# Kernel optimization log

Hardware: AMD Instinct MI355X
Metric: run time of the kernel (lower is better)

The kernel has to match this reference:

```python
import jax, jax.numpy as jnp
import numpy as np

T = 16384
D = 2048      # input_dim
H = 256       # gru hidden
NF = 8        # n_frames (top-k)
NC = 2        # n_classes


def _gru_dir(x_gates, W_hh, b_hh, reverse):
    # x_gates: (T, 3H) precomputed input projection; torch gate order: r, z, n
    def step(h, gx):
        gh = h @ W_hh.T + b_hh
        xr, xz, xn = jnp.split(gx, 3)
        hr, hz, hn = jnp.split(gh, 3)
        r = jax.nn.sigmoid(xr + hr)
        z = jax.nn.sigmoid(xz + hz)
        n = jnp.tanh(xn + r * hn)
        h_new = (1.0 - z) * n + z * h
        return h_new, h_new
    h0 = jnp.zeros((W_hh.shape[1],), x_gates.dtype)
    _, hs = jax.lax.scan(step, h0, x_gates, reverse=reverse)
    return hs  # (T, H)


def setup_inputs() -> dict:
    key = jax.random.key(0)
    ks = jax.random.split(key, 16)
    s = 0.02
    inp = {
        "features": jax.random.normal(ks[0], (T, D), jnp.float32),
        "temperature": jnp.float32(0.5),
        # BiGRU params (torch layout: W_ih (3H, D), W_hh (3H, H))
        "W_ih_f": jax.random.normal(ks[1], (3 * H, D), jnp.float32) * s,
        "W_hh_f": jax.random.normal(ks[2], (3 * H, H), jnp.float32) * s,
        "b_ih_f": jnp.zeros((3 * H,), jnp.float32),
        "b_hh_f": jnp.zeros((3 * H,), jnp.float32),
        "W_ih_b": jax.random.normal(ks[3], (3 * H, D), jnp.float32) * s,
        "W_hh_b": jax.random.normal(ks[4], (3 * H, H), jnp.float32) * s,
        "b_ih_b": jnp.zeros((3 * H,), jnp.float32),
        "b_hh_b": jnp.zeros((3 * H,), jnp.float32),
        # scorer MLP: Linear(2H,64) -> ReLU -> Linear(64,1)
        "Ws1": jax.random.normal(ks[5], (64, 2 * H), jnp.float32) * s,
        "bs1": jnp.zeros((64,), jnp.float32),
        "Ws2": jax.random.normal(ks[6], (1, 64), jnp.float32) * s,
        "bs2": jnp.zeros((1,), jnp.float32),
        # classifier: Linear(D,256) -> ReLU -> Linear(256,NC)
        "Wc1": jax.random.normal(ks[7], (256, D), jnp.float32) * s,
        "bc1": jnp.zeros((256,), jnp.float32),
        "Wc2": jax.random.normal(ks[8], (NC, 256), jnp.float32) * s,
        "bc2": jnp.zeros((NC,), jnp.float32),
    }
    return inp


def reference(features, temperature, W_ih_f, W_hh_f, b_ih_f, b_hh_f,
              W_ih_b, W_hh_b, b_ih_b, b_hh_b, Ws1, bs1, Ws2, bs2,
              Wc1, bc1, Wc2, bc2):
    # FrameScorer: BiGRU
    gx_f = features @ W_ih_f.T + b_ih_f            # (T, 3H)
    gx_b = features @ W_ih_b.T + b_ih_b
    h_f = _gru_dir(gx_f, W_hh_f, b_hh_f, reverse=False)
    h_b = _gru_dir(gx_b, W_hh_b, b_hh_b, reverse=True)
    h = jnp.concatenate([h_f, h_b], axis=-1)       # (T, 2H)
    # scorer MLP (dropout is identity in eval)
    scores = (jax.nn.relu(h @ Ws1.T + bs1) @ Ws2.T + bs2)[:, 0]   # (T,)
    # soft top-k weights
    n = min(NF, scores.shape[0])
    _, topk_idx = jax.lax.top_k(scores, n)
    mask = jnp.zeros_like(scores).at[topk_idx].set(1.0)
    masked_scores = scores * mask + (1.0 - mask) * (-1e9)
    weights = jax.nn.softmax(masked_scores / temperature)          # (T,)
    # weighted feature sum + classifier
    clip_repr = weights @ features                                  # (D,)
    logits = jax.nn.relu(clip_repr @ Wc1.T + bc1) @ Wc2.T + bc2     # (NC,)
    return logits, scores
```

## Files before the change

### kernel.cpp

```cpp
#include <hip/hip_runtime.h>
#include <hip/hip_fp16.h>
#include <math.h>

#define T_LEN 16384
#define D_IN  2048
#define H_GRU 256
#define G3    768
#define NFRM  8
#define NCLS  2

#define CHUNK 32
#define WARM  48
#define GSTEPS (WARM + CHUNK)
#define BQ    4
#define NCHUNK (T_LEN / CHUNK)
#define GRU_BLOCKS (NCHUNK / BQ)

typedef _Float16 f16x8 __attribute__((ext_vector_type(8)));
typedef float    f32x4 __attribute__((ext_vector_type(4)));

static const size_t OFF_GXF = 0;
static const size_t OFF_GXB = OFF_GXF + (size_t)T_LEN * G3;
static const size_t OFF_H   = OFF_GXB + (size_t)T_LEN * G3;
static const size_t OFF_BIA = OFF_H   + (size_t)T_LEN * 512;
static const size_t OFF_SC  = OFF_BIA + 2 * G3;
static const size_t OFF_WPF = OFF_SC  + (size_t)T_LEN;
static const size_t OFF_WPB = OFF_WPF + (size_t)G3 * H_GRU / 2;
static const size_t OFF_SEL = OFF_WPB + (size_t)G3 * H_GRU / 2;
static const size_t OFF_CH  = OFF_SEL + 16;

__device__ __forceinline__ float fsig(float x) {
    return __builtin_amdgcn_rcpf(1.f + __expf(-x));
}
__device__ __forceinline__ float ftanh(float x) {
    float e = __expf(2.f * x);
    return 1.f - 2.f * __builtin_amdgcn_rcpf(e + 1.f);
}

__global__ void bias_fold_kernel(const float* __restrict__ bi0, const float* __restrict__ bh0,
                                 const float* __restrict__ bi1, const float* __restrict__ bh1,
                                 float* __restrict__ o0, float* __restrict__ o1) {
    int t = blockIdx.x * 256 + threadIdx.x;
    if (t < G3) {
        float a0 = bi0[t], a1 = bi1[t];
        if (t < 512) { a0 += bh0[t]; a1 += bh1[t]; }
        o0[t] = a0; o1[t] = a1;
    }
}

__global__ void pack_whh_mfma_kernel(const float* __restrict__ W0,
                                     const float* __restrict__ W1,
                                     f16x8* __restrict__ P0,
                                     f16x8* __restrict__ P1) {
    const float* W = blockIdx.y ? W1 : W0;
    f16x8* P = blockIdx.y ? P1 : P0;
    int tc = blockIdx.x;
    int l = threadIdx.x;
    int t = tc >> 3, c = tc & 7;
    int m = t * 16 + (l & 15);
    int k = c * 32 + (l >> 4) * 8;
    const float* src = W + (size_t)m * H_GRU + k;
    f16x8 v;
#pragma unroll
    for (int j = 0; j < 8; ++j) v[j] = (_Float16)src[j];
    P[(size_t)tc * 64 + l] = v;
}

#define GM 128
#define GN 128
#define GK 32
__global__ __launch_bounds__(256, 2) void gemm_f16_kernel(
    const float* __restrict__ A,
    const float* __restrict__ B0, const float* __restrict__ B1,
    const float* __restrict__ bias0, const float* __restrict__ bias1,
    float* __restrict__ C0, float* __restrict__ C1,
    int M, int N, int K) {
    const float* __restrict__ B    = blockIdx.z ? B1 : B0;
    const float* __restrict__ bias = blockIdx.z ? bias1 : bias0;
    float* __restrict__ C          = blockIdx.z ? C1 : C0;

    __shared__ __align__(16) __half As[GM][GK];
    __shared__ __align__(16) __half Bs[GN][GK];

    const int tid  = threadIdx.x;
    const int bm   = blockIdx.x * GM;
    const int bn   = blockIdx.y * GN;
    const int lane = tid & 63;
    const int wave = tid >> 6;
    const int mw   = wave & 1;
    const int nw   = wave >> 1;
    const int lm   = lane & 15;
    const int lk   = lane >> 4;

    const int srow = tid >> 3;
    const int scol = (tid & 7) * 4;

    f32x4 acc[4][4];
#pragma unroll
    for (int a = 0; a < 4; ++a)
#pragma unroll
        for (int b = 0; b < 4; ++b) acc[a][b] = (f32x4)0.f;

    for (int k0 = 0; k0 < K; k0 += GK) {
        float4 av[4], bv[4];
#pragma unroll
        for (int j = 0; j < 4; ++j) {
            av[j] = *(const float4*)&A[(size_t)(bm + 32 * j + srow) * K + k0 + scol];
            bv[j] = *(const float4*)&B[(size_t)(bn + 32 * j + srow) * K + k0 + scol];
        }
        __syncthreads();
#pragma unroll
        for (int j = 0; j < 4; ++j) {
            int r = 32 * j + srow;
            *((__half2*)&As[r][scol + 0]) = __float22half2_rn(make_float2(av[j].x, av[j].y));
            *((__half2*)&As[r][scol + 2]) = __float22half2_rn(make_float2(av[j].z, av[j].w));
            *((__half2*)&Bs[r][scol + 0]) = __float22half2_rn(make_float2(bv[j].x, bv[j].y));
            *((__half2*)&Bs[r][scol + 2]) = __float22half2_rn(make_float2(bv[j].z, bv[j].w));
        }
        __syncthreads();

        f16x8 afr[4], bfr[4];
#pragma unroll
        for (int tm = 0; tm < 4; ++tm)
            afr[tm] = *(const f16x8*)&As[64 * mw + 16 * tm + lm][lk * 8];
#pragma unroll
        for (int tn = 0; tn < 4; ++tn)
            bfr[tn] = *(const f16x8*)&Bs[64 * nw + 16 * tn + lm][lk * 8];
#pragma unroll
        for (int tm = 0; tm < 4; ++tm)
#pragma unroll
            for (int tn = 0; tn < 4; ++tn)
                acc[tm][tn] = __builtin_amdgcn_mfma_f32_16x16x32_f16(
                    afr[tm], bfr[tn], acc[tm][tn], 0, 0, 0);
    }

#pragma unroll
    for (int tm = 0; tm < 4; ++tm) {
#pragma unroll
        for (int tn = 0; tn < 4; ++tn) {
            int gn = bn + 64 * nw + 16 * tn + lm;
            float bb = bias[gn];
#pragma unroll
            for (int reg = 0; reg < 4; ++reg) {
                int gm = bm + 64 * mw + 16 * tm + lk * 4 + reg;
                C[(size_t)gm * N + gn] = acc[tm][tn][reg] + bb;
            }
        }
    }
}

#define BM 64
#define BN 64
#define BK 32
__global__ __launch_bounds__(256) void scorer_kernel(
    const float* __restrict__ A,
    const float* __restrict__ B,
    const float* __restrict__ bias,
    const float* __restrict__ Ws2,
    const float* __restrict__ bs2,
    float* __restrict__ sc, float* __restrict__ outs,
    int M, int N, int K) {
    __shared__ __align__(16) float As[BK][BM + 4];
    __shared__ __align__(16) float Bs[BK][BN + 4];

    const int tid = threadIdx.x;
    const int bm = blockIdx.x * BM;
    const int kk8 = tid & 7;
    const int r32 = tid >> 3;
    const int tx = tid & 15;
    const int ty = tid >> 4;

    float acc[4][4];
#pragma unroll
    for (int a = 0; a < 4; ++a)
#pragma unroll
        for (int b = 0; b < 4; ++b) acc[a][b] = 0.f;

    for (int k0 = 0; k0 < K; k0 += BK) {
        float4 a0 = *(const float4*)&A[(size_t)(bm + r32) * K + k0 + kk8 * 4];
        float4 a1 = *(const float4*)&A[(size_t)(bm + r32 + 32) * K + k0 + kk8 * 4];
        float4 b0 = *(const float4*)&B[(size_t)(r32) * K + k0 + kk8 * 4];
        float4 b1 = *(const float4*)&B[(size_t)(r32 + 32) * K + k0 + kk8 * 4];
        __syncthreads();
        As[kk8 * 4 + 0][r32] = a0.x; As[kk8 * 4 + 1][r32] = a0.y;
        As[kk8 * 4 + 2][r32] = a0.z; As[kk8 * 4 + 3][r32] = a0.w;
        As[kk8 * 4 + 0][r32 + 32] = a1.x; As[kk8 * 4 + 1][r32 + 32] = a1.y;
        As[kk8 * 4 + 2][r32 + 32] = a1.z; As[kk8 * 4 + 3][r32 + 32] = a1.w;
        Bs[kk8 * 4 + 0][r32] = b0.x; Bs[kk8 * 4 + 1][r32] = b0.y;
        Bs[kk8 * 4 + 2][r32] = b0.z; Bs[kk8 * 4 + 3][r32] = b0.w;
        Bs[kk8 * 4 + 0][r32 + 32] = b1.x; Bs[kk8 * 4 + 1][r32 + 32] = b1.y;
        Bs[kk8 * 4 + 2][r32 + 32] = b1.z; Bs[kk8 * 4 + 3][r32 + 32] = b1.w;
        __syncthreads();
#pragma unroll 8
        for (int kk = 0; kk < BK; ++kk) {
            float4 av = *(const float4*)&As[kk][ty * 4];
            float4 bv = *(const float4*)&Bs[kk][tx * 4];
            acc[0][0] += av.x * bv.x; acc[0][1] += av.x * bv.y; acc[0][2] += av.x * bv.z; acc[0][3] += av.x * bv.w;
            acc[1][0] += av.y * bv.x; acc[1][1] += av.y * bv.y; acc[1][2] += av.y * bv.z; acc[1][3] += av.y * bv.w;
            acc[2][0] += av.z * bv.x; acc[2][1] += av.z * bv.y; acc[2][2] += av.z * bv.z; acc[2][3] += av.z * bv.w;
            acc[3][0] += av.w * bv.x; acc[3][1] += av.w * bv.y; acc[3][2] += av.w * bv.z; acc[3][3] += av.w * bv.w;
        }
    }

    float4 bvv = *(const float4*)&bias[tx * 4];
    float4 w2  = *(const float4*)&Ws2[tx * 4];
    const float b2 = bs2[0];
#pragma unroll
    for (int im = 0; im < 4; ++im) {
        float s = fmaxf(acc[im][0] + bvv.x, 0.f) * w2.x
                + fmaxf(acc[im][1] + bvv.y, 0.f) * w2.y
                + fmaxf(acc[im][2] + bvv.z, 0.f) * w2.z
                + fmaxf(acc[im][3] + bvv.w, 0.f) * w2.w;
#pragma unroll
        for (int off = 1; off < 16; off <<= 1) s += __shfl_xor(s, off);
        if (tx == 0) {
            int m = bm + ty * 4 + im;
            float sval = s + b2;
            sc[m] = sval;
            outs[m] = sval;
        }
    }
}

#define HPAD 272
__global__ __launch_bounds__(1024, 4) void gru_v5_kernel(
    const float* __restrict__ gx0, const float* __restrict__ gx1,
    const f16x8* __restrict__ Wk0, const f16x8* __restrict__ Wk1,
    const float* __restrict__ bh0, const float* __restrict__ bh1,
    float* __restrict__ Hbuf) {
    const int dir = blockIdx.y;
    const float* __restrict__ gx = dir ? gx1 : gx0;
    const f16x8* __restrict__ Wk = dir ? Wk1 : Wk0;
    const float* __restrict__ bh = dir ? bh1 : bh0;
    const int col_off = dir * 256;

    const int tid  = threadIdx.x;
    const int lane = tid & 63;
    const int wv   = tid >> 6;
    const int ln   = lane & 15;
    const int lq   = lane >> 4;

    __shared__ __align__(16) __half h_sh[16][HPAD];
    __shared__ __align__(16) float red[4][772];

    f16x8 Wf[3][8];
#pragma unroll
    for (int tt = 0; tt < 3; ++tt)
#pragma unroll
        for (int c = 0; c < 8; ++c)
            Wf[tt][c] = Wk[(size_t)((3 * wv + tt) * 8 + c) * 64 + lane];

    for (int idx = tid; idx < 16 * HPAD; idx += 1024) ((__half*)h_sh)[idx] = __float2half(0.f);

    const int i   = tid & 255;
    const int grp = tid >> 8;
    const float bn_ = bh[512 + i];
    float h_own = 0.f;
    const int cbase = blockIdx.x * BQ;
    const int dtv = dir ? -1 : 1;
    const int lo = (cbase + grp) * CHUNK;
    const int t0 = dir ? (lo + CHUNK - 1 + WARM) : (lo - WARM);
    __syncthreads();

    for (int s = 0; s < GSTEPS; ++s) {
        const int t = t0 + dtv * s;
        const bool valid = ((unsigned)t < (unsigned)T_LEN);
        const int tc2 = t < 0 ? 0 : (t > T_LEN - 1 ? T_LEN - 1 : t);
        const float* g = gx + (size_t)tc2 * G3 + i;
        const float xr = g[0], xz = g[256], xn = g[512];

        f32x4 acc[3];
#pragma unroll
        for (int tt = 0; tt < 3; ++tt) acc[tt] = (f32x4)0.f;
#pragma unroll
        for (int c = 0; c < 8; ++c) {
            f16x8 bfr = *(const f16x8*)&h_sh[ln][c * 32 + lq * 8];
#pragma unroll
            for (int tt = 0; tt < 3; ++tt)
                acc[tt] = __builtin_amdgcn_mfma_f32_16x16x32_f16(Wf[tt][c], bfr, acc[tt], 0, 0, 0);
        }
        if (ln < 4) {
#pragma unroll
            for (int tt = 0; tt < 3; ++tt)
                *(f32x4*)&red[ln][(3 * wv + tt) * 16 + lq * 4] = acc[tt];
        }
        __syncthreads();

        const float r = fsig(xr + red[grp][i]);
        const float z = fsig(xz + red[grp][256 + i]);
        const float nn = ftanh(xn + r * (red[grp][512 + i] + bn_));
        const float hnew = (1.f - z) * nn + z * h_own;
        if (valid) {
            h_own = hnew;
            h_sh[grp][i] = __float2half(hnew);
            const bool pay = dir ? (t < lo + CHUNK) : (t >= lo);
            if (pay) Hbuf[(size_t)t * 512 + col_off + i] = hnew;
        }
        __syncthreads();
    }
}

__global__ __launch_bounds__(256) void select_topk_kernel(
    const float* __restrict__ scores, const float* __restrict__ temp_p,
    int* __restrict__ sel_idx_out, float* __restrict__ sel_w_out) {
    __shared__ float red_v[4];
    __shared__ int   red_i[4];
    __shared__ int   bcast_idx;
    __shared__ int   sel_idx_sh[NFRM];
    __shared__ float sel_v_sh[NFRM];

    const int tid  = threadIdx.x;
    const int lane = tid & 63;
    const int wv   = tid >> 6;

    float sv[64];
#pragma unroll
    for (int a = 0; a < 64; ++a) sv[a] = scores[a * 256 + tid];

    for (int round = 0; round < NFRM; ++round) {
        float best = -1e30f;
        int bidx = 0x7fffffff;
#pragma unroll
        for (int a = 0; a < 64; ++a) {
            if (sv[a] > best) { best = sv[a]; bidx = a * 256 + tid; }
        }
#pragma unroll
        for (int off = 32; off > 0; off >>= 1) {
            float v2 = __shfl_down(best, off);
            int   i2 = __shfl_down(bidx, off);
            if (v2 > best || (v2 == best && i2 < bidx)) { best = v2; bidx = i2; }
        }
        if (lane == 0) { red_v[wv] = best; red_i[wv] = bidx; }
        __syncthreads();
        if (tid == 0) {
            float bv = red_v[0]; int bi = red_i[0];
#pragma unroll
            for (int w = 1; w < 4; ++w)
                if (red_v[w] > bv || (red_v[w] == bv && red_i[w] < bi)) { bv = red_v[w]; bi = red_i[w]; }
            sel_idx_sh[round] = bi; sel_v_sh[round] = bv; bcast_idx = bi;
        }
        __syncthreads();
        const int widx = bcast_idx;
        if ((widx & 255) == tid) {
            const int aa = widx >> 8;
#pragma unroll
            for (int a = 0; a < 64; ++a)
                if (a == aa) sv[a] = -1e30f;
        }
    }

    if (tid == 0) {
        float temp = temp_p[0];
        float m = sel_v_sh[0];
        float e[NFRM];
        float sum = 0.f;
        for (int j = 0; j < NFRM; ++j) { e[j] = expf((sel_v_sh[j] - m) / temp); sum += e[j]; }
        for (int j = 0; j < NFRM; ++j) { sel_idx_out[j] = sel_idx_sh[j]; sel_w_out[j] = e[j] / sum; }
    }
}

__global__ __launch_bounds__(256) void classifier1_kernel(
    const float* __restrict__ features,
    const int* __restrict__ sel_idx, const float* __restrict__ sel_w,
    const float* __restrict__ Wc1, const float* __restrict__ bc1,
    float* __restrict__ hid) {
    const int r = blockIdx.x;
    const int tid = threadIdx.x;
    __shared__ int   s_idx[NFRM];
    __shared__ float s_w[NFRM];
    __shared__ float part[4];
    if (tid < NFRM) { s_idx[tid] = sel_idx[tid]; s_w[tid] = sel_w[tid]; }
    __syncthreads();

    float acc = 0.f;
#pragma unroll
    for (int q = 0; q < D_IN / 256; ++q) {
        int d = q * 256 + tid;
        float c = 0.f;
#pragma unroll
        for (int j = 0; j < NFRM; ++j)
            c += s_w[j] * features[(size_t)s_idx[j] * D_IN + d];
        acc += c * Wc1[(size_t)r * D_IN + d];
    }
#pragma unroll
    for (int off = 32; off > 0; off >>= 1) acc += __shfl_down(acc, off);
    if ((tid & 63) == 0) part[tid >> 6] = acc;
    __syncthreads();
    if (tid == 0)
        hid[r] = fmaxf(part[0] + part[1] + part[2] + part[3] + bc1[r], 0.f);
}

__global__ __launch_bounds__(128) void classifier2_kernel(
    const float* __restrict__ hid, const float* __restrict__ Wc2,
    const float* __restrict__ bc2, float* __restrict__ out) {
    const int tid = threadIdx.x;
    const int c = tid >> 6;
    const int l = tid & 63;
    float acc = 0.f;
#pragma unroll
    for (int k = l; k < 256; k += 64) acc += hid[k] * Wc2[c * 256 + k];
#pragma unroll
    for (int off = 32; off > 0; off >>= 1) acc += __shfl_down(acc, off);
    if (l == 0) out[c] = acc + bc2[c];
}

extern "C" void kernel_launch(void* const* d_in, const int* in_sizes, int n_in,
                              void* d_out, int out_size, void* d_ws, size_t ws_size,
                              hipStream_t stream) {
    const float* features = (const float*)d_in[0];
    const float* temperature = (const float*)d_in[1];
    const float* W_ih_f = (const float*)d_in[2];
    const float* W_hh_f = (const float*)d_in[3];
    const float* b_ih_f = (const float*)d_in[4];
    const float* b_hh_f = (const float*)d_in[5];
    const float* W_ih_b = (const float*)d_in[6];
    const float* W_hh_b = (const float*)d_in[7];
    const float* b_ih_b = (const float*)d_in[8];
    const float* b_hh_b = (const float*)d_in[9];
    const float* Ws1 = (const float*)d_in[10];
    const float* bs1 = (const float*)d_in[11];
    const float* Ws2 = (const float*)d_in[12];
    const float* bs2 = (const float*)d_in[13];
    const float* Wc1 = (const float*)d_in[14];
    const float* bc1 = (const float*)d_in[15];
    const float* Wc2 = (const float*)d_in[16];
    const float* bc2 = (const float*)d_in[17];

    float* ws = (float*)d_ws;
    float* gx_f = ws + OFF_GXF;
    float* gx_b = ws + OFF_GXB;
    float* Hbuf = ws + OFF_H;
    float* biaf = ws + OFF_BIA;
    float* biab = ws + OFF_BIA + G3;
    float* sc   = ws + OFF_SC;
    f16x8* Wk_f = (f16x8*)(ws + OFF_WPF);
    f16x8* Wk_b = (f16x8*)(ws + OFF_WPB);
    int*   sel_i = (int*)(ws + OFF_SEL);
    float* sel_w = ws + OFF_SEL + NFRM;
    float* chid  = ws + OFF_CH;
    float* out  = (float*)d_out;

    bias_fold_kernel<<<3, 256, 0, stream>>>(b_ih_f, b_hh_f, b_ih_b, b_hh_b, biaf, biab);

    pack_whh_mfma_kernel<<<dim3(384, 2), 64, 0, stream>>>(W_hh_f, W_hh_b, Wk_f, Wk_b);

    gemm_f16_kernel<<<dim3(T_LEN / GM, G3 / GN, 2), 256, 0, stream>>>(
        features, W_ih_f, W_ih_b, biaf, biab, gx_f, gx_b, T_LEN, G3, D_IN);

    gru_v5_kernel<<<dim3(GRU_BLOCKS, 2), 1024, 0, stream>>>(
        gx_f, gx_b, Wk_f, Wk_b, b_hh_f, b_hh_b, Hbuf);

    scorer_kernel<<<T_LEN / BM, 256, 0, stream>>>(
        Hbuf, Ws1, bs1, Ws2, bs2, sc, out + 2, T_LEN, 64, 512);

    select_topk_kernel<<<1, 256, 0, stream>>>(sc, temperature, sel_i, sel_w);

    classifier1_kernel<<<256, 256, 0, stream>>>(features, sel_i, sel_w, Wc1, bc1, chid);

    classifier2_kernel<<<1, 128, 0, stream>>>(chid, Wc2, bc2, out);
}
```

Before: 591.4 us.

## Restructure input-projection GEMM with direct-to-LDS loads and pre-converted fp16 weights

Pre-converts both W_ih matrices to fp16 once, into scratch space later reused for the hidden buffer. The input-projection GEMM now uses global_load_lds to move tiles straight into shared memory, stores A as fp32 in LDS and converts it to fp16 in registers. Both directions run in a single swizzled 1D grid so blocks that share feature rows are scheduled close together for L2 reuse. This removes register staging and halves B-tile traffic, at the cost of an extra conversion kernel, doubled LDS footprint for A, and no register prefetch overlap within the K loop.

```diff
diff --git a/kernel.cpp b/kernel.cpp
--- a/kernel.cpp
+++ b/kernel.cpp
@@ -37,6 +37,22 @@
     return 1.f - 2.f * __builtin_amdgcn_rcpf(e + 1.f);
 }
 
+__device__ __forceinline__ void gload_lds16(const void* gp, void* lp) {
+    __builtin_amdgcn_global_load_lds(
+        (const __attribute__((address_space(1))) void*)gp,
+        (__attribute__((address_space(3))) void*)lp,
+        16, 0, 0);
+}
+
+__device__ __forceinline__ f16x8 pack8(const f32x4 lo, const f32x4 hi) {
+    f16x8 r;
+    r[0] = (_Float16)lo[0]; r[1] = (_Float16)lo[1];
+    r[2] = (_Float16)lo[2]; r[3] = (_Float16)lo[3];
+    r[4] = (_Float16)hi[0]; r[5] = (_Float16)hi[1];
+    r[6] = (_Float16)hi[2]; r[7] = (_Float16)hi[3];
+    return r;
+}
+
 __global__ void bias_fold_kernel(const float* __restrict__ bi0, const float* __restrict__ bh0,
                                  const float* __restrict__ bi1, const float* __restrict__ bh1,
                                  float* __restrict__ o0, float* __restrict__ o1) {
@@ -46,6 +62,22 @@
         if (t < 512) { a0 += bh0[t]; a1 += bh1[t]; }
         o0[t] = a0; o1[t] = a1;
     }
+}
+
+__global__ __launch_bounds__(256) void cvt_w_kernel(const float* __restrict__ Wf,
+                                                    const float* __restrict__ Wb,
+                                                    __half* __restrict__ B16) {
+    const float* __restrict__ src = blockIdx.y ? Wb : Wf;
+    __half* __restrict__ dst = B16 + (size_t)blockIdx.y * G3 * D_IN;
+    const int i = blockIdx.x * 256 + threadIdx.x;
+    float4 a = *(const float4*)&src[(size_t)i * 8];
+    float4 b = *(const float4*)&src[(size_t)i * 8 + 4];
+    __half2 h[4];
+    h[0] = __float22half2_rn(make_float2(a.x, a.y));
+    h[1] = __float22half2_rn(make_float2(a.z, a.w));
+    h[2] = __float22half2_rn(make_float2(b.x, b.y));
+    h[3] = __float22half2_rn(make_float2(b.z, b.w));
+    *(float4*)&dst[(size_t)i * 8] = *(float4*)h;
 }
 
 __global__ void pack_whh_mfma_kernel(const float* __restrict__ W0,
@@ -66,34 +98,38 @@
     P[(size_t)tc * 64 + l] = v;
 }
 
-#define GM 128
-#define GN 128
-#define GK 32
-__global__ __launch_bounds__(256, 2) void gemm_f16_kernel(
+#define GXBK 32
+__global__ __launch_bounds__(256) void gemm_gx_kernel(
     const float* __restrict__ A,
-    const float* __restrict__ B0, const float* __restrict__ B1,
-    const float* __restrict__ bias0, const float* __restrict__ bias1,
-    float* __restrict__ C0, float* __restrict__ C1,
-    int M, int N, int K) {
-    const float* __restrict__ B    = blockIdx.z ? B1 : B0;
-    const float* __restrict__ bias = blockIdx.z ? bias1 : bias0;
-    float* __restrict__ C          = blockIdx.z ? C1 : C0;
-
-    __shared__ __align__(16) __half As[GM][GK];
-    __shared__ __align__(16) __half Bs[GN][GK];
+    const __half* __restrict__ B16,
+    const float* __restrict__ biaf, const float* __restrict__ biab,
+    float* __restrict__ Cf, float* __restrict__ Cb) {
+    __shared__ __align__(16) float  Asf[4096];
+    __shared__ __align__(16) __half Bsh[4096];
 
     const int tid  = threadIdx.x;
-    const int bm   = blockIdx.x * GM;
-    const int bn   = blockIdx.y * GN;
     const int lane = tid & 63;
     const int wave = tid >> 6;
+    const int lm   = lane & 15;
+    const int lk   = lane >> 4;
     const int mw   = wave & 1;
     const int nw   = wave >> 1;
-    const int lm   = lane & 15;
-    const int lk   = lane >> 4;
-
-    const int srow = tid >> 3;
-    const int scol = (tid & 7) * 4;
+
+    const int wg = blockIdx.x;
+    const int id = (wg & 7) * (1536 / 8) + (wg >> 3);
+    const int mt = id / 12;
+    const int nt = id - mt * 12;
+    const int bm  = mt * 128;
+    const int bnt = nt * 128;
+
+    const float* __restrict__ bias;
+    float* __restrict__ C;
+    int bn_local;
+    if (nt < 6) { C = Cf; bias = biaf; bn_local = bnt; }
+    else        { C = Cb; bias = biab; bn_local = bnt - 768; }
+
+    const float*  gA = A   + (size_t)(bm  + lm) * D_IN + lk * 8;
+    const __half* gB = B16 + (size_t)(bnt + lm) * D_IN + lk * 8;
 
     f32x4 acc[4][4];
 #pragma unroll
@@ -101,31 +137,33 @@
 #pragma unroll
         for (int b = 0; b < 4; ++b) acc[a][b] = (f32x4)0.f;
 
-    for (int k0 = 0; k0 < K; k0 += GK) {
-        float4 av[4], bv[4];
+    for (int k0 = 0; k0 < D_IN; k0 += GXBK) {
+        __syncthreads();
 #pragma unroll
         for (int j = 0; j < 4; ++j) {
-            av[j] = *(const float4*)&A[(size_t)(bm + 32 * j + srow) * K + k0 + scol];
-            bv[j] = *(const float4*)&B[(size_t)(bn + 32 * j + srow) * K + k0 + scol];
-        }
-        __syncthreads();
-#pragma unroll
-        for (int j = 0; j < 4; ++j) {
-            int r = 32 * j + srow;
-            *((__half2*)&As[r][scol + 0]) = __float22half2_rn(make_float2(av[j].x, av[j].y));
-            *((__half2*)&As[r][scol + 2]) = __float22half2_rn(make_float2(av[j].z, av[j].w));
-            *((__half2*)&Bs[r][scol + 0]) = __float22half2_rn(make_float2(bv[j].x, bv[j].y));
-            *((__half2*)&Bs[r][scol + 2]) = __float22half2_rn(make_float2(bv[j].z, bv[j].w));
+            const int q = 4 * wave + j, f = q >> 1, h = q & 1;
+            gload_lds16(gA + (size_t)(16 * f) * D_IN + k0 + 4 * h, &Asf[q * 256]);
+        }
+#pragma unroll
+        for (int j = 0; j < 2; ++j) {
+            const int f = 2 * wave + j;
+            gload_lds16(gB + (size_t)(16 * f) * D_IN + k0, &Bsh[f * 512]);
         }
         __syncthreads();
 
         f16x8 afr[4], bfr[4];
 #pragma unroll
-        for (int tm = 0; tm < 4; ++tm)
-            afr[tm] = *(const f16x8*)&As[64 * mw + 16 * tm + lm][lk * 8];
-#pragma unroll
-        for (int tn = 0; tn < 4; ++tn)
-            bfr[tn] = *(const f16x8*)&Bs[64 * nw + 16 * tn + lm][lk * 8];
+        for (int tm = 0; tm < 4; ++tm) {
+            const int q0 = (4 * mw + tm) * 2;
+            f32x4 lo = *(const f32x4*)&Asf[q0 * 256 + lane * 4];
+            f32x4 hi = *(const f32x4*)&Asf[q0 * 256 + 256 + lane * 4];
+            afr[tm] = pack8(lo, hi);
+        }
+#pragma unroll
+        for (int tn = 0; tn < 4; ++tn) {
+            const int fb = 4 * nw + tn;
+            bfr[tn] = *(const f16x8*)&Bsh[fb * 512 + lane * 8];
+        }
 #pragma unroll
         for (int tm = 0; tm < 4; ++tm)
 #pragma unroll
@@ -138,12 +176,12 @@
     for (int tm = 0; tm < 4; ++tm) {
 #pragma unroll
         for (int tn = 0; tn < 4; ++tn) {
-            int gn = bn + 64 * nw + 16 * tn + lm;
+            int gn = bn_local + 64 * nw + 16 * tn + lm;
             float bb = bias[gn];
 #pragma unroll
             for (int reg = 0; reg < 4; ++reg) {
                 int gm = bm + 64 * mw + 16 * tm + lk * 4 + reg;
-                C[(size_t)gm * N + gn] = acc[tm][tn][reg] + bb;
+                C[(size_t)gm * G3 + gn] = acc[tm][tn][reg] + bb;
             }
         }
     }
@@ -440,12 +478,15 @@
     float* chid  = ws + OFF_CH;
     float* out  = (float*)d_out;
 
+    __half* B16 = (__half*)(ws + OFF_H);
+
     bias_fold_kernel<<<3, 256, 0, stream>>>(b_ih_f, b_hh_f, b_ih_b, b_hh_b, biaf, biab);
 
+    cvt_w_kernel<<<dim3(768, 2), 256, 0, stream>>>(W_ih_f, W_ih_b, B16);
+
     pack_whh_mfma_kernel<<<dim3(384, 2), 64, 0, stream>>>(W_hh_f, W_hh_b, Wk_f, Wk_b);
 
-    gemm_f16_kernel<<<dim3(T_LEN / GM, G3 / GN, 2), 256, 0, stream>>>(
-        features, W_ih_f, W_ih_b, biaf, biab, gx_f, gx_b, T_LEN, G3, D_IN);
+    gemm_gx_kernel<<<1536, 256, 0, stream>>>(features, B16, biaf, biab, gx_f, gx_b);
 
     gru_v5_kernel<<<dim3(GRU_BLOCKS, 2), 1024, 0, stream>>>(
         gx_f, gx_b, Wk_f, Wk_b, b_hh_f, b_hh_b, Hbuf);
```

Result: slower. 703.7 us (+19.0%).
